# Performance work log

Hardware: AMD Instinct MI355X
Metric: run time of the kernel (lower is better)

The kernel has to match this reference:

```python
import jax, jax.numpy as jnp
import numpy as np

N = 256       # ImageSize
NC = 8        # coils
NSPOKE = 34   # radial spokes
NVEC = 512    # samples per spoke
M = NSPOKE * NVEC


def setup_inputs() -> dict:
    key = jax.random.key(0)
    k1, k2, k3, k4 = jax.random.split(key, 4)
    X = jax.random.normal(k1, (N, N, 2), dtype=jnp.float32)
    # nonuniform k-space coordinates in [-pi, pi)
    angles = (jax.random.uniform(k2, (M, 2), dtype=jnp.float32) * 2.0 - 1.0) * jnp.pi
    C = jax.random.normal(k3, (NC, N, N, 2), dtype=jnp.float32)   # coil sensitivities (re/im)
    w = jax.random.uniform(k4, (NSPOKE, NVEC), dtype=jnp.float32)  # density compensation
    return {"X": X, "angles": angles, "C": C, "w": w,
            "Nspoke": NSPOKE, "Nvec": NVEC, "Nc": NC}


def _forward(X, angles, C, w, Nspoke, Nvec, Nc):
    # X: (N,N,2) real/imag image; C: (Nc,N,N,2); angles: (M,2); w: (Nspoke,Nvec)
    n = X.shape[0]
    # uniform grid coords; N even -> linspace(-N//2, N//2-1, N) == arange
    x = jnp.arange(-(n // 2), n - (n // 2), dtype=jnp.float32)  # (N,)
    img = (X[..., 0] + 1j * X[..., 1]).astype(jnp.complex64)    # (N,N)
    Cc = (C[..., 0] + 1j * C[..., 1]).astype(jnp.complex64)     # (Nc,N,N)
    src = img[None] * Cc                                        # coil images (Nc,N,N)
    s = angles[:, 0]
    t = angles[:, 1]
    # Type-3 NUFFT as separable direct DFT: y[c,k] = sum_{a,b} src[c,a,b] e^{-i(s_k x_a + t_k x_b)}
    Ea = jnp.exp((-1j) * s[:, None] * x[None, :]).astype(jnp.complex64)  # (M,N)
    Eb = jnp.exp((-1j) * t[:, None] * x[None, :]).astype(jnp.complex64)  # (M,N)
    tmp = jnp.einsum('cab,kb->cka', src, Eb)   # (Nc,M,N) -- dominant intermediate
    y = jnp.einsum('cka,ka->ck', tmp, Ea)      # (Nc,M)
    yc = y.reshape(Nc, Nspoke, Nvec) * w       # density compensation
    y = yc.reshape(Nc, Nspoke * Nvec)
    return jnp.stack([y.real, y.imag], axis=-1)  # (Nc, M, 2) float32


def reference(X, angles, C, w, Nspoke, Nvec, Nc):
    return _forward(X, angles, C, w, Nspoke, Nvec, Nc)
```

## Files before the change

kernel.cpp:

```cpp
#include <hip/hip_runtime.h>

#define NC   8
#define MTOT 17408

typedef __attribute__((ext_vector_type(8))) short short8;
typedef __attribute__((ext_vector_type(4))) float f32x4;

typedef __attribute__((address_space(3))) unsigned       lds_uint;
typedef const __attribute__((address_space(1))) unsigned glb_uint;

static __device__ __forceinline__ short f2bf(float f) {
    union { float f; unsigned u; } v; v.f = f;
    return (short)((v.u + 0x7fffu + ((v.u >> 16) & 1u)) >> 16);
}

__global__ __launch_bounds__(256) void build_src(
        const float* __restrict__ X, const float* __restrict__ C,
        short* __restrict__ Sr, short* __restrict__ Si) {
    int idx = blockIdx.x * 256 + threadIdx.x;
    int ab = idx & 65535;
    float xr = X[ab * 2 + 0], xi = X[ab * 2 + 1];
    float cr = C[idx * 2 + 0], ci = C[idx * 2 + 1];
    Sr[idx] = f2bf(xr * cr - xi * ci);
    Si[idx] = f2bf(xr * ci + xi * cr);
}

__global__ __launch_bounds__(256) void nufft_fwd(
        const float* __restrict__ angles, const float* __restrict__ w,
        const short* __restrict__ SrP, const short* __restrict__ SiP,
        float* __restrict__ out) {
    __shared__ char lds[32768];

    const int lane = threadIdx.x & 63;
    const int wv   = threadIdx.x >> 6;
    const int c    = blockIdx.y;
    const int col  = lane & 15;
    const int grp  = lane >> 4;
    const int kglob = blockIdx.x * 64 + wv * 16 + col;

    const float s = angles[kglob * 2 + 0];
    const float t = angles[kglob * 2 + 1];

    const short* Sr = SrP + c * 65536;
    const short* Si = SiP + c * 65536;

    short8 Br[8], Bi[8];
    #pragma unroll
    for (int bs = 0; bs < 8; ++bs) {
        short8 re, im;
        #pragma unroll
        for (int j = 0; j < 8; ++j) {
            float xb = (float)(bs * 32 + grp * 8 + j - 128);
            float sn, cs;
            __sincosf(t * xb, &sn, &cs);
            re[j] = f2bf(cs);
            im[j] = f2bf(-sn);
        }
        Br[bs] = re; Bi[bs] = im;
    }

    auto stage = [&](int at, int half) {
        #pragma unroll
        for (int it = 0; it < 4; ++it) {
            int L   = it * 256 + wv * 64 + lane;
            int row = (L >> 5) & 15;
            int cb  = (L & 31) ^ (row & 7);
            const short* g = ((L >> 9) ? Si : Sr) + (at * 16 + row) * 256 + cb * 8;
            __builtin_amdgcn_global_load_lds(
                (glb_uint*)g,
                (lds_uint*)(lds + half * 16384 + it * 4096 + wv * 1024),
                16, 0, 0);
        }
    };

    float yr = 0.f, yi = 0.f;

    stage(0, 0);
    __syncthreads();

    for (int at = 0; at < 16; ++at) {
        const int cur = at & 1;
        if (at < 15) stage(at + 1, cur ^ 1);

        const char* buf = lds + cur * 16384;
        f32x4 P1 = {0.f,0.f,0.f,0.f}, P2 = {0.f,0.f,0.f,0.f};
        f32x4 P3 = {0.f,0.f,0.f,0.f}, P4 = {0.f,0.f,0.f,0.f};
        const int rowoff = col * 512;
        const int swz    = col & 7;
        #pragma unroll
        for (int bs = 0; bs < 8; ++bs) {
            int cbp = ((grp | (bs << 2)) ^ swz) << 4;
            short8 Arf = *(const short8*)(buf + rowoff + cbp);
            short8 Aif = *(const short8*)(buf + 8192 + rowoff + cbp);
            P1 = __builtin_amdgcn_mfma_f32_16x16x32_bf16(Arf, Br[bs], P1, 0, 0, 0);
            P2 = __builtin_amdgcn_mfma_f32_16x16x32_bf16(Aif, Bi[bs], P2, 0, 0, 0);
            P3 = __builtin_amdgcn_mfma_f32_16x16x32_bf16(Arf, Bi[bs], P3, 0, 0, 0);
            P4 = __builtin_amdgcn_mfma_f32_16x16x32_bf16(Aif, Br[bs], P4, 0, 0, 0);
        }
        int a0 = at * 16 + grp * 4;
        #pragma unroll
        for (int r = 0; r < 4; ++r) {
            float Tr = P1[r] - P2[r];
            float Ti = P3[r] + P4[r];
            float sn, cs;
            __sincosf(s * (float)(a0 + r - 128), &sn, &cs);
            yr += cs * Tr + sn * Ti;
            yi += cs * Ti - sn * Tr;
        }
        __syncthreads();
    }

    yr += __shfl_xor(yr, 16); yr += __shfl_xor(yr, 32);
    yi += __shfl_xor(yi, 16); yi += __shfl_xor(yi, 32);

    if (grp == 0) {
        float wk = w[kglob];
        out[(c * MTOT + kglob) * 2 + 0] = yr * wk;
        out[(c * MTOT + kglob) * 2 + 1] = yi * wk;
    }
}

extern "C" void kernel_launch(void* const* d_in, const int* in_sizes, int n_in,
                              void* d_out, int out_size, void* d_ws, size_t ws_size,
                              hipStream_t stream) {
    const float* X      = (const float*)d_in[0];
    const float* angles = (const float*)d_in[1];
    const float* C      = (const float*)d_in[2];
    const float* w      = (const float*)d_in[3];
    float* out = (float*)d_out;

    short* Sr = (short*)d_ws;
    short* Si = Sr + NC * 65536;

    build_src<<<dim3(NC * 65536 / 256), dim3(256), 0, stream>>>(X, C, Sr, Si);

    dim3 grid(MTOT / 64, NC);
    nufft_fwd<<<grid, dim3(256), 0, stream>>>(angles, w, Sr, Si, out);
}
```

Baseline: 90.22 us.

## Switch to 32x32x16 MFMA tiles and precompute Eb table once per k

The main kernel moves from 16x16x32 to 32x32x16 bf16 MFMA, so each wave handles 32 k-samples and each LDS stage holds 32 image rows, with the LDS buffer doubled to 64KB. A separate kernel builds the bf16 Eb sincos table once, so it is no longer recomputed for each of the 8 coil blocks. If the workspace is too small, the code falls back to computing the table inside the kernel. The change adds a kernel launch and extra global traffic for the table, and the larger LDS footprint may limit occupancy.

```diff
diff --git a/kernel.cpp b/kernel.cpp
--- a/kernel.cpp
+++ b/kernel.cpp
@@ -3,8 +3,8 @@
 #define NC   8
 #define MTOT 17408
 
-typedef __attribute__((ext_vector_type(8))) short short8;
-typedef __attribute__((ext_vector_type(4))) float f32x4;
+typedef __attribute__((ext_vector_type(8)))  short short8;
+typedef __attribute__((ext_vector_type(16))) float f32x16;
 
 typedef __attribute__((address_space(3))) unsigned       lds_uint;
 typedef const __attribute__((address_space(1))) unsigned glb_uint;
@@ -25,50 +25,84 @@
     Si[idx] = f2bf(xr * ci + xi * cr);
 }
 
-__global__ __launch_bounds__(256) void nufft_fwd(
+__global__ __launch_bounds__(256) void build_ebt(
+        const float* __restrict__ angles, short* __restrict__ EbT) {
+    int gid  = blockIdx.x * 256 + threadIdx.x;
+    int kt   = gid >> 10;
+    int r    = gid & 1023;
+    int ks   = r >> 6;
+    int lane = r & 63;
+    int k    = kt * 32 + (lane & 31);
+    float t  = angles[k * 2 + 1];
+    short8 re, im;
+    #pragma unroll
+    for (int j = 0; j < 8; ++j) {
+        float xb = (float)(ks * 16 + (lane >> 5) * 8 + j - 128);
+        float sn, cs;
+        __sincosf(t * xb, &sn, &cs);
+        re[j] = f2bf(cs);
+        im[j] = f2bf(-sn);
+    }
+    short* base = EbT + (size_t)(kt * 32 + ks) * 512 + lane * 8;
+    *(short8*)(base)        = re;
+    *(short8*)(base + 8192) = im;
+}
+
+template<int USE_TABLE>
+__global__ __launch_bounds__(256, 2) void nufft_fwd(
         const float* __restrict__ angles, const float* __restrict__ w,
         const short* __restrict__ SrP, const short* __restrict__ SiP,
-        float* __restrict__ out) {
-    __shared__ char lds[32768];
+        const short* __restrict__ EbT, float* __restrict__ out) {
+    __shared__ char lds[65536];
 
-    const int lane = threadIdx.x & 63;
-    const int wv   = threadIdx.x >> 6;
+    const int tid  = threadIdx.x;
+    const int lane = tid & 63;
+    const int wv   = tid >> 6;
     const int c    = blockIdx.y;
-    const int col  = lane & 15;
-    const int grp  = lane >> 4;
-    const int kglob = blockIdx.x * 64 + wv * 16 + col;
-
-    const float s = angles[kglob * 2 + 0];
-    const float t = angles[kglob * 2 + 1];
+    const int col  = lane & 31;
+    const int hi   = lane >> 5;
+    const int kt   = blockIdx.x * 4 + wv;
+    const int k    = kt * 32 + col;
+    const float s  = angles[k * 2 + 0];
 
     const short* Sr = SrP + c * 65536;
     const short* Si = SiP + c * 65536;
 
-    short8 Br[8], Bi[8];
-    #pragma unroll
-    for (int bs = 0; bs < 8; ++bs) {
-        short8 re, im;
+    short8 Br[16], Bi[16];
+    if constexpr (USE_TABLE) {
+        const short* tb = EbT + (size_t)(kt * 32) * 512 + lane * 8;
         #pragma unroll
-        for (int j = 0; j < 8; ++j) {
-            float xb = (float)(bs * 32 + grp * 8 + j - 128);
-            float sn, cs;
-            __sincosf(t * xb, &sn, &cs);
-            re[j] = f2bf(cs);
-            im[j] = f2bf(-sn);
+        for (int ks = 0; ks < 16; ++ks) {
+            Br[ks] = *(const short8*)(tb + ks * 512);
+            Bi[ks] = *(const short8*)(tb + 8192 + ks * 512);
         }
-        Br[bs] = re; Bi[bs] = im;
+    } else {
+        const float t = angles[k * 2 + 1];
+        #pragma unroll
+        for (int ks = 0; ks < 16; ++ks) {
+            short8 re, im;
+            #pragma unroll
+            for (int j = 0; j < 8; ++j) {
+                float xb = (float)(ks * 16 + hi * 8 + j - 128);
+                float sn, cs;
+                __sincosf(t * xb, &sn, &cs);
+                re[j] = f2bf(cs);
+                im[j] = f2bf(-sn);
+            }
+            Br[ks] = re; Bi[ks] = im;
+        }
     }
 
     auto stage = [&](int at, int half) {
         #pragma unroll
-        for (int it = 0; it < 4; ++it) {
-            int L   = it * 256 + wv * 64 + lane;
-            int row = (L >> 5) & 15;
+        for (int it = 0; it < 8; ++it) {
+            int L   = it * 256 + tid;
+            int row = (L >> 5) & 31;
             int cb  = (L & 31) ^ (row & 7);
-            const short* g = ((L >> 9) ? Si : Sr) + (at * 16 + row) * 256 + cb * 8;
+            const short* g = ((L >> 10) ? Si : Sr) + (at * 32 + row) * 256 + cb * 8;
             __builtin_amdgcn_global_load_lds(
                 (glb_uint*)g,
-                (lds_uint*)(lds + half * 16384 + it * 4096 + wv * 1024),
+                (lds_uint*)(lds + half * 32768 + (it * 256 + (tid & ~63)) * 16),
                 16, 0, 0);
         }
     };
@@ -78,45 +112,44 @@
     stage(0, 0);
     __syncthreads();
 
-    for (int at = 0; at < 16; ++at) {
+    for (int at = 0; at < 8; ++at) {
         const int cur = at & 1;
-        if (at < 15) stage(at + 1, cur ^ 1);
+        if (at < 7) stage(at + 1, cur ^ 1);
 
-        const char* buf = lds + cur * 16384;
-        f32x4 P1 = {0.f,0.f,0.f,0.f}, P2 = {0.f,0.f,0.f,0.f};
-        f32x4 P3 = {0.f,0.f,0.f,0.f}, P4 = {0.f,0.f,0.f,0.f};
+        const char* buf = lds + cur * 32768;
+        f32x16 P1 = {0.f}, P2 = {0.f}, P3 = {0.f}, P4 = {0.f};
         const int rowoff = col * 512;
         const int swz    = col & 7;
         #pragma unroll
-        for (int bs = 0; bs < 8; ++bs) {
-            int cbp = ((grp | (bs << 2)) ^ swz) << 4;
-            short8 Arf = *(const short8*)(buf + rowoff + cbp);
-            short8 Aif = *(const short8*)(buf + 8192 + rowoff + cbp);
-            P1 = __builtin_amdgcn_mfma_f32_16x16x32_bf16(Arf, Br[bs], P1, 0, 0, 0);
-            P2 = __builtin_amdgcn_mfma_f32_16x16x32_bf16(Aif, Bi[bs], P2, 0, 0, 0);
-            P3 = __builtin_amdgcn_mfma_f32_16x16x32_bf16(Arf, Bi[bs], P3, 0, 0, 0);
-            P4 = __builtin_amdgcn_mfma_f32_16x16x32_bf16(Aif, Br[bs], P4, 0, 0, 0);
+        for (int ks = 0; ks < 16; ++ks) {
+            int slot = ((ks * 2 + hi) ^ swz) << 4;
+            short8 Arf = *(const short8*)(buf + rowoff + slot);
+            short8 Aif = *(const short8*)(buf + 16384 + rowoff + slot);
+            P1 = __builtin_amdgcn_mfma_f32_32x32x16_bf16(Arf, Br[ks], P1, 0, 0, 0);
+            P2 = __builtin_amdgcn_mfma_f32_32x32x16_bf16(Aif, Bi[ks], P2, 0, 0, 0);
+            P3 = __builtin_amdgcn_mfma_f32_32x32x16_bf16(Arf, Bi[ks], P3, 0, 0, 0);
+            P4 = __builtin_amdgcn_mfma_f32_32x32x16_bf16(Aif, Br[ks], P4, 0, 0, 0);
         }
-        int a0 = at * 16 + grp * 4;
         #pragma unroll
-        for (int r = 0; r < 4; ++r) {
-            float Tr = P1[r] - P2[r];
-            float Ti = P3[r] + P4[r];
+        for (int reg = 0; reg < 16; ++reg) {
+            int ap = at * 32 + (reg & 3) + 8 * (reg >> 2) + 4 * hi - 128;
+            float Tr = P1[reg] - P2[reg];
+            float Ti = P3[reg] + P4[reg];
             float sn, cs;
-            __sincosf(s * (float)(a0 + r - 128), &sn, &cs);
+            __sincosf(s * (float)ap, &sn, &cs);
             yr += cs * Tr + sn * Ti;
             yi += cs * Ti - sn * Tr;
         }
         __syncthreads();
     }
 
-    yr += __shfl_xor(yr, 16); yr += __shfl_xor(yr, 32);
-    yi += __shfl_xor(yi, 16); yi += __shfl_xor(yi, 32);
+    yr += __shfl_xor(yr, 32);
+    yi += __shfl_xor(yi, 32);
 
-    if (grp == 0) {
-        float wk = w[kglob];
-        out[(c * MTOT + kglob) * 2 + 0] = yr * wk;
-        out[(c * MTOT + kglob) * 2 + 1] = yi * wk;
+    if (hi == 0) {
+        float wk = w[k];
+        out[((size_t)c * MTOT + k) * 2 + 0] = yr * wk;
+        out[((size_t)c * MTOT + k) * 2 + 1] = yi * wk;
     }
 }
 
@@ -129,11 +162,20 @@
     const float* w      = (const float*)d_in[3];
     float* out = (float*)d_out;
 
-    short* Sr = (short*)d_ws;
-    short* Si = Sr + NC * 65536;
+    short* Sr  = (short*)d_ws;
+    short* Si  = Sr + NC * 65536;
+    short* EbT = Si + NC * 65536;
+
+    size_t need = ((size_t)NC * 65536 * 2 + (size_t)MTOT * 512) * sizeof(short);
+    const bool use_table = ws_size >= need;
 
     build_src<<<dim3(NC * 65536 / 256), dim3(256), 0, stream>>>(X, C, Sr, Si);
 
-    dim3 grid(MTOT / 64, NC);
-    nufft_fwd<<<grid, dim3(256), 0, stream>>>(angles, w, Sr, Si, out);
+    dim3 grid(MTOT / 128, NC);
+    if (use_table) {
+        build_ebt<<<dim3(MTOT * 32 / 256), dim3(256), 0, stream>>>(angles, EbT);
+        nufft_fwd<1><<<grid, dim3(256), 0, stream>>>(angles, w, Sr, Si, EbT, out);
+    } else {
+        nufft_fwd<0><<<grid, dim3(256), 0, stream>>>(angles, w, Sr, Si, nullptr, out);
+    }
 }
```

New measurement: 96.52 us. +7.0%, slower.
